# Performance work log

Measured on AMD Instinct MI355X. Metric: run time of the kernel, lower is better.

Reference implementation:

```python
import jax, jax.numpy as jnp
import numpy as np

N_WAY = 5
K_SHOT = 5
NBNN_TOPK = 3
TEMPERATURE = 2.0
EPS = 1e-8


def setup_inputs() -> dict:
    key = jax.random.key(0)
    k1, k2, k3 = jax.random.split(key, 3)
    b, q, c, h, w = 4, 75, 640, 11, 11
    s = N_WAY * K_SHOT
    support_xf = jax.random.normal(k1, (b, s, c, h, w), jnp.float32)
    query_xf = jax.random.normal(k2, (b, q, c, h, w), jnp.float32)
    # episodes are ordered class-major: [way0 shots..., way1 shots..., ...]
    support_y = jnp.tile(jnp.repeat(jnp.arange(N_WAY, dtype=jnp.int32), K_SHOT)[None, :], (b, 1))
    query_y = jax.random.randint(k3, (b, q), 0, N_WAY, dtype=jnp.int32)
    return {"support_xf": support_xf, "query_xf": query_xf,
            "support_y": support_y, "query_y": query_y}


def _mn4_loss(support_xf, query_xf, query_y):
    b, s, c, h, w = support_xf.shape
    q = query_xf.shape[1]
    M_q = h * w
    M_s = K_SHOT * h * w

    # ---- InnerproductSimilarity (cosine) ----
    # support: [b, N, c, M_s]  (class-major grouping of shots)
    sf = support_xf.reshape(b, N_WAY, K_SHOT, c, h * w).transpose(0, 1, 3, 2, 4).reshape(b, N_WAY, c, M_s)
    qf = query_xf.reshape(b, q, c, M_q)
    sf = sf / (jnp.linalg.norm(sf, axis=2, keepdims=True) + EPS)
    qf = qf / (jnp.linalg.norm(qf, axis=2, keepdims=True) + EPS)
    # simi: [b, q, N, M_q, M_s]
    simi = jnp.einsum('bqcm,bncs->bqnms', qf, sf)

    # ---- _MNN (compensate_for_single=True branch) ----
    # merged view: [b, q, M_q, N*M_s]
    merged = simi.transpose(0, 1, 3, 2, 4).reshape(b, q, M_q, N_WAY * M_s)
    query_nearest = jnp.argmax(merged, axis=-1)          # [b, q, M_q]
    class_wise_max = simi.max(-1).max(2) + 1.0           # [b, q, M_q]
    class_m = jax.nn.one_hot(query_nearest, N_WAY * M_s, dtype=simi.dtype) * class_wise_max[..., None]
    support_nearest = jnp.argmax(class_m, axis=-2)       # [b, q, N*M_s]
    gathered = jnp.take_along_axis(support_nearest, query_nearest, axis=-1)  # [b, q, M_q]
    q_mask = (gathered == jnp.arange(M_q)[None, None, :])                    # [b, q, M_q]

    # ---- NBNN value: topk over support descriptors, masked sum over query descriptors ----
    topv = jax.lax.top_k(simi, NBNN_TOPK)[0].mean(-1)    # [b, q, N, M_q]
    query_value = (topv * q_mask[:, :, None, :].astype(topv.dtype)).sum(-1)  # [b, q, N]
    logits = query_value.reshape(b * q, N_WAY) / TEMPERATURE

    # ---- cross entropy (mean) ----
    logp = jax.nn.log_softmax(logits, axis=-1)
    y = query_y.reshape(-1)
    loss = -jnp.take_along_axis(logp, y[:, None], axis=1).mean()
    return loss


def reference(support_xf, query_xf, support_y, query_y):
    del support_y  # episodes are class-major by construction
    return _mn4_loss(support_xf, query_xf, query_y)
```

## Files before the change

### kernel.cpp

```cpp
#include <hip/hip_runtime.h>
#include <hip/hip_bf16.h>
#include <math.h>

#define BB 4
#define QQ 75
#define NBQ 300
#define CC 640
#define HW 121
#define NW 5
#define KS 5
#define SS 25
#define MS 605
#define JT 3025
#define BQ_PER_XCD 38

typedef __attribute__((ext_vector_type(8))) short short8;
typedef __attribute__((ext_vector_type(4))) float f32x4;

#define OFF_SBF   0
#define SBF_F     (BB*JT*CC/2)
#define OFF_QBF   (OFF_SBF + SBF_F)
#define QBF_F     (NBQ*HW*CC/2)
#define OFF_P     (OFF_QBF + QBF_F)

__device__ __forceinline__ void async16(const void* g, void* l) {
    __builtin_amdgcn_global_load_lds(
        (const __attribute__((address_space(1))) unsigned int*)g,
        (__attribute__((address_space(3))) unsigned int*)l, 16, 0, 0);
}

__global__ void prep_kernel(const float* __restrict__ sup, const float* __restrict__ qry,
                            __hip_bfloat16* __restrict__ Sbf, __hip_bfloat16* __restrict__ Qbf,
                            float* __restrict__ out)
{
    const int col = blockIdx.x;
    const int t   = threadIdx.x;
    if (col == 0 && t == 0) out[0] = 0.f;
    const float* src;
    __hip_bfloat16* dst;
    if (col < BB * SS) {
        const int b = col / SS, s = col % SS;
        const int n = s / KS, k = s % KS;
        src = sup + (size_t)col * (CC * HW);
        dst = Sbf + ((size_t)b * JT + n * MS + k * HW) * CC;
    } else {
        const int bq = col - BB * SS;
        src = qry + (size_t)bq * (CC * HW);
        dst = Qbf + (size_t)bq * (HW * CC);
    }

    __shared__ float inv[128];
    __shared__ float T[32][128];

    const int cc2 = t >> 7, hw1 = t & 127;
    float ss0 = 0.f, ss1 = 0.f;
    if (hw1 < HW) {
        const float* p = src + hw1;
#pragma unroll 16
        for (int c = cc2; c < CC; c += 4) {
            float v0 = p[(size_t)c * HW];
            float v1 = p[(size_t)(c + 2) * HW];
            ss0 = fmaf(v0, v0, ss0);
            ss1 = fmaf(v1, v1, ss1);
        }
    }
    T[cc2][hw1] = ss0 + ss1;
    __syncthreads();
    if (t < 128) inv[t] = (t < HW) ? 1.f / (sqrtf(T[0][t] + T[1][t]) + 1e-8f) : 0.f;

    for (int c0 = 0; c0 < CC; c0 += 32) {
        __syncthreads();
#pragma unroll
        for (int i = 0; i < 16; ++i) {
            int idx = t + i * 256;
            int cc = idx >> 7, hw = idx & 127;
            if (hw < HW) T[cc][hw] = src[(size_t)(c0 + cc) * HW + hw] * inv[hw];
        }
        __syncthreads();
        const int hw = t >> 1, half = t & 1;
        if (hw < HW) {
            __hip_bfloat16 hv[16];
#pragma unroll
            for (int i = 0; i < 16; ++i) hv[i] = __float2bfloat16(T[half * 16 + i][hw]);
            int4* op = reinterpret_cast<int4*>(dst + (size_t)hw * CC + c0 + half * 16);
            op[0] = reinterpret_cast<int4*>(hv)[0];
            op[1] = reinterpret_cast<int4*>(hv)[1];
        }
    }
}

__launch_bounds__(256, 2)
__global__ void simi_kernel(const __hip_bfloat16* __restrict__ Sbf,
                            const __hip_bfloat16* __restrict__ Qbf,
                            float4* __restrict__ pout)
{
    const int xcd   = blockIdx.x & 7;
    const int local = blockIdx.x >> 3;
    const int n     = local % NW;
    const int bq    = xcd * BQ_PER_XCD + local / NW;
    if (bq >= NBQ) return;
    const int b   = bq / QQ;
    const int tid = threadIdx.x;
    const int lane = tid & 63, wid = tid >> 6;
    const int l15 = lane & 15, l4 = lane >> 4;
    const int wr0 = (wid & 1) * 64;
    const int wc0 = (wid >> 1) * 64;

    const unsigned short* qbase = (const unsigned short*)(Qbf + (size_t)bq * (HW * CC));
    const unsigned short* sbase = (const unsigned short*)(Sbf + ((size_t)b * JT + n * MS) * CC);

    __shared__ __align__(16) unsigned short AsBuf[2][128 * 64];
    __shared__ __align__(16) unsigned short BsBuf[2][128 * 64];

    const int srow = lane >> 3;
    const int kb   = (lane & 7) ^ srow;
    int aoff[4];
#pragma unroll
    for (int p = 0; p < 4; ++p) {
        int arow = wid * 32 + p * 8 + srow;
        int grow = arow < HW ? arow : HW - 1;
        aoff[p] = grow * CC + kb * 8;
    }
    const int ldso_base = wid * 4096 + lane * 16;

#define STAGE(ms0_, c0_, nb_)                                                        \
    {                                                                                \
        _Pragma("unroll")                                                            \
        for (int p = 0; p < 4; ++p) {                                                \
            const int ldso = ldso_base + p * 1024;                                   \
            async16(qbase + aoff[p] + (c0_), (char*)&AsBuf[nb_][0] + ldso);          \
            int j_ = (ms0_) + wid * 32 + p * 8 + srow;                               \
            int jc_ = j_ < MS ? j_ : MS - 1;                                         \
            async16(sbase + jc_ * CC + kb * 8 + (c0_), (char*)&BsBuf[nb_][0] + ldso);\
        }                                                                            \
    }

    float rt0[16], rt1[16], rt2[16]; int ra[16];
#pragma unroll
    for (int i = 0; i < 16; ++i) { rt0[i] = -INFINITY; rt1[i] = -INFINITY; rt2[i] = -INFINITY; ra[i] = 0; }

    f32x4 acc[4][4];
#pragma unroll
    for (int mi = 0; mi < 4; ++mi)
#pragma unroll
        for (int ni = 0; ni < 4; ++ni)
#pragma unroll
            for (int r = 0; r < 4; ++r) acc[mi][ni][r] = 0.f;

    STAGE(0, 0, 0);
    int nb = 0;

    for (int t = 0; t < 50; ++t) {
        const int tn = t + 1;
        if (tn < 50) {
            const int nms = (tn / 10) * 128;
            const int nc  = (tn % 10) * 64;
            STAGE(nms, nc, nb ^ 1);
            asm volatile("s_waitcnt vmcnt(8)" ::: "memory");
        } else {
            asm volatile("s_waitcnt vmcnt(0)" ::: "memory");
        }
        __builtin_amdgcn_s_barrier();

#pragma unroll
        for (int ks = 0; ks < 2; ++ks) {
            const int slot = (ks * 4 + l4) ^ (l15 & 7);
            short8 af[4], bf[4];
#pragma unroll
            for (int mi = 0; mi < 4; ++mi)
                af[mi] = *(const short8*)(&AsBuf[nb][0] + (wr0 + mi * 16 + l15) * 64 + slot * 8);
#pragma unroll
            for (int ni = 0; ni < 4; ++ni)
                bf[ni] = *(const short8*)(&BsBuf[nb][0] + (wc0 + ni * 16 + l15) * 64 + slot * 8);
#pragma unroll
            for (int mi = 0; mi < 4; ++mi)
#pragma unroll
                for (int ni = 0; ni < 4; ++ni)
                    acc[mi][ni] = __builtin_amdgcn_mfma_f32_16x16x32_bf16(
                        af[mi], bf[ni], acc[mi][ni], 0, 0, 0);
        }
        nb ^= 1;

        if ((t % 10) == 9) {
            const int ms0 = (t / 10) * 128;
            int jg[4]; bool jvalid[4];
#pragma unroll
            for (int nf = 0; nf < 4; ++nf) {
                const int jl = ms0 + wc0 + nf * 16 + l15;
                jvalid[nf] = (jl < MS);
                jg[nf] = n * MS + jl;
            }
#pragma unroll
            for (int mi = 0; mi < 4; ++mi)
#pragma unroll
                for (int nf = 0; nf < 4; ++nf)
#pragma unroll
                    for (int r = 0; r < 4; ++r) {
                        const int si = mi * 4 + r;
                        float v = jvalid[nf] ? acc[mi][nf][r] : -INFINITY;
                        const bool gt = v > rt0[si];
                        ra[si] = gt ? jg[nf] : ra[si];
                        const float m1 = fminf(rt0[si], v);
                        rt0[si] = fmaxf(rt0[si], v);
                        const float m2 = fminf(rt1[si], m1);
                        rt1[si] = fmaxf(rt1[si], m1);
                        rt2[si] = fmaxf(rt2[si], m2);
                    }
#pragma unroll
            for (int mi = 0; mi < 4; ++mi)
#pragma unroll
                for (int ni = 0; ni < 4; ++ni)
#pragma unroll
                    for (int r = 0; r < 4; ++r) acc[mi][ni][r] = 0.f;
        }

        __builtin_amdgcn_s_barrier();
    }

#pragma unroll
    for (int si = 0; si < 16; ++si) {
#pragma unroll
        for (int mask = 1; mask <= 8; mask <<= 1) {
            const float o0 = __shfl_xor(rt0[si], mask);
            const float o1 = __shfl_xor(rt1[si], mask);
            const float o2 = __shfl_xor(rt2[si], mask);
            const int   oa = __shfl_xor(ra[si],  mask);
            const bool take = (o0 > rt0[si]) || (o0 == rt0[si] && oa < ra[si]);
            ra[si] = take ? oa : ra[si];
            float m1 = fminf(rt0[si], o0); rt0[si] = fmaxf(rt0[si], o0);
            float m2 = fminf(rt1[si], m1); rt1[si] = fmaxf(rt1[si], m1);
            rt2[si] = fmaxf(rt2[si], m2);
            m1 = fminf(rt0[si], o1); rt0[si] = fmaxf(rt0[si], o1);
            m2 = fminf(rt1[si], m1); rt1[si] = fmaxf(rt1[si], m1);
            rt2[si] = fmaxf(rt2[si], m2);
            m1 = fminf(rt0[si], o2); rt0[si] = fmaxf(rt0[si], o2);
            m2 = fminf(rt1[si], m1); rt1[si] = fmaxf(rt1[si], m1);
            rt2[si] = fmaxf(rt2[si], m2);
        }
    }

    float s0 = rt0[0], s1 = rt1[0], s2 = rt2[0]; int sa = ra[0];
#pragma unroll
    for (int i = 1; i < 16; ++i) {
        const bool p = (l15 == i);
        s0 = p ? rt0[i] : s0; s1 = p ? rt1[i] : s1; s2 = p ? rt2[i] : s2; sa = p ? ra[i] : sa;
    }
    const int m = wr0 + (l15 >> 2) * 16 + l4 * 4 + (l15 & 3);

    __syncthreads();
    float4* mbuf = (float4*)&AsBuf[0][0];
    if ((wid >> 1) == 0) {
        float4 v; v.x = s0; v.y = s1; v.z = s2; v.w = __int_as_float(sa);
        mbuf[m] = v;
    }
    __syncthreads();
    if ((wid >> 1) == 1) {
        const float4 o = mbuf[m];
        const int oa = __float_as_int(o.w);
        const bool take = (o.x > s0) || (o.x == s0 && oa < sa);
        sa = take ? oa : sa;
        float m1 = fminf(s0, o.x); s0 = fmaxf(s0, o.x);
        float m2 = fminf(s1, m1);  s1 = fmaxf(s1, m1);
        s2 = fmaxf(s2, m2);
        m1 = fminf(s0, o.y); s0 = fmaxf(s0, o.y);
        m2 = fminf(s1, m1);  s1 = fmaxf(s1, m1);
        s2 = fmaxf(s2, m2);
        m1 = fminf(s0, o.z); s0 = fmaxf(s0, o.z);
        m2 = fminf(s1, m1);  s1 = fmaxf(s1, m1);
        s2 = fmaxf(s2, m2);
        if (m < HW) {
            float4 v; v.x = s0; v.y = s1; v.z = s2; v.w = __int_as_float(sa);
            pout[(bq * NW + n) * HW + m] = v;
        }
    }
#undef STAGE
}

__global__ void merge_kernel(const float4* __restrict__ pout, const int* __restrict__ qy,
                             float* __restrict__ out)
{
    const int bq  = blockIdx.x;
    const int tid = threadIdx.x;

    __shared__ float cw[128];
    __shared__ int   ag[128];
    __shared__ float tv[NW][128];
    __shared__ float maskf[128];
    __shared__ float lg[8];

    if (tid < HW) {
        float g0 = -INFINITY; int garg = 0;
#pragma unroll
        for (int n = 0; n < NW; ++n) {
            const float4 a = pout[(bq * NW + n) * HW + tid];
            if (a.x > g0) { g0 = a.x; garg = __float_as_int(a.w); }
            tv[n][tid] = (a.x + a.y + a.z) * (1.f / 3.f);
        }
        cw[tid] = g0 + 1.0f;
        ag[tid] = garg;
    }
    __syncthreads();
    if (tid < HW) {
        const float mycw = cw[tid];
        const int   myag = ag[tid];
        float ok = 1.f;
        for (int m2 = 0; m2 < HW; ++m2) {
            if (m2 == tid) continue;
            if (ag[m2] == myag) {
                float c2 = cw[m2];
                if (c2 > mycw || (c2 == mycw && m2 < tid)) ok = 0.f;
            }
        }
        maskf[tid] = ok;
    }
    __syncthreads();
    if (tid < NW) {
        float s = 0.f;
        for (int mq = 0; mq < HW; ++mq) s += maskf[mq] * tv[tid][mq];
        lg[tid] = s * 0.5f;
    }
    __syncthreads();
    if (tid == 0) {
        float m = lg[0];
#pragma unroll
        for (int n2 = 1; n2 < NW; ++n2) m = fmaxf(m, lg[n2]);
        float se = 0.f;
#pragma unroll
        for (int n2 = 0; n2 < NW; ++n2) se += expf(lg[n2] - m);
        int y = qy[bq];
        atomicAdd(out, -(lg[y] - m - logf(se)) * (1.f / NBQ));
    }
}

extern "C" void kernel_launch(void* const* d_in, const int* in_sizes, int n_in,
                              void* d_out, int out_size, void* d_ws, size_t ws_size,
                              hipStream_t stream)
{
    const float* sup = (const float*)d_in[0];
    const float* qry = (const float*)d_in[1];
    const int*   qy  = (const int*)d_in[3];
    float* out = (float*)d_out;
    float* ws  = (float*)d_ws;

    __hip_bfloat16* Sbf = (__hip_bfloat16*)(ws + OFF_SBF);
    __hip_bfloat16* Qbf = (__hip_bfloat16*)(ws + OFF_QBF);
    float4* pout = (float4*)(ws + OFF_P);

    hipLaunchKernelGGL(prep_kernel, dim3(BB * SS + NBQ), dim3(256), 0, stream,
                       sup, qry, Sbf, Qbf, out);
    hipLaunchKernelGGL(simi_kernel, dim3(8 * BQ_PER_XCD * NW), dim3(256), 0, stream,
                       Sbf, Qbf, pout);
    hipLaunchKernelGGL(merge_kernel, dim3(NBQ), dim3(128), 0, stream, pout, qy, out);
}
```

Before: 406.1 us.

## Halve simi K-tile to 32, raise occupancy to 3 blocks, add MFMA priority

```diff
diff --git a/kernel.cpp b/kernel.cpp
--- a/kernel.cpp
+++ b/kernel.cpp
@@ -74,7 +74,7 @@
         for (int i = 0; i < 16; ++i) {
             int idx = t + i * 256;
             int cc = idx >> 7, hw = idx & 127;
-            if (hw < HW) T[cc][hw] = src[(size_t)(c0 + cc) * HW + hw] * inv[hw];
+            if (hw < 128 && hw < HW) T[cc][hw] = src[(size_t)(c0 + cc) * HW + hw] * inv[hw];
         }
         __syncthreads();
         const int hw = t >> 1, half = t & 1;
@@ -89,7 +89,7 @@
     }
 }
 
-__launch_bounds__(256, 2)
+__launch_bounds__(256, 3)
 __global__ void simi_kernel(const __hip_bfloat16* __restrict__ Sbf,
                             const __hip_bfloat16* __restrict__ Qbf,
                             float4* __restrict__ pout)
@@ -109,27 +109,31 @@
     const unsigned short* qbase = (const unsigned short*)(Qbf + (size_t)bq * (HW * CC));
     const unsigned short* sbase = (const unsigned short*)(Sbf + ((size_t)b * JT + n * MS) * CC);
 
-    __shared__ __align__(16) unsigned short AsBuf[2][128 * 64];
-    __shared__ __align__(16) unsigned short BsBuf[2][128 * 64];
-
-    const int srow = lane >> 3;
-    const int kb   = (lane & 7) ^ srow;
-    int aoff[4];
-#pragma unroll
-    for (int p = 0; p < 4; ++p) {
-        int arow = wid * 32 + p * 8 + srow;
+    __shared__ __align__(16) unsigned short AsBuf[2][128 * 32];
+    __shared__ __align__(16) unsigned short BsBuf[2][128 * 32];
+
+    const int srow = lane >> 2;
+    const int kb   = (lane & 3) ^ ((lane >> 3) & 3);
+    int aoff2[2];
+#pragma unroll
+    for (int g = 0; g < 2; ++g) {
+        int arow = wid * 32 + g * 16 + srow;
         int grow = arow < HW ? arow : HW - 1;
-        aoff[p] = grow * CC + kb * 8;
-    }
-    const int ldso_base = wid * 4096 + lane * 16;
+        aoff2[g] = grow * CC + kb * 8;
+    }
+    int jb2[2];
+#pragma unroll
+    for (int g = 0; g < 2; ++g) jb2[g] = wid * 32 + g * 16 + srow;
+
+    const int ldso_base = wid * 2048 + lane * 16;
 
 #define STAGE(ms0_, c0_, nb_)                                                        \
     {                                                                                \
         _Pragma("unroll")                                                            \
-        for (int p = 0; p < 4; ++p) {                                                \
-            const int ldso = ldso_base + p * 1024;                                   \
-            async16(qbase + aoff[p] + (c0_), (char*)&AsBuf[nb_][0] + ldso);          \
-            int j_ = (ms0_) + wid * 32 + p * 8 + srow;                               \
+        for (int g = 0; g < 2; ++g) {                                                \
+            const int ldso = ldso_base + g * 1024;                                   \
+            async16(qbase + aoff2[g] + (c0_), (char*)&AsBuf[nb_][0] + ldso);         \
+            int j_ = (ms0_) + jb2[g];                                                \
             int jc_ = j_ < MS ? j_ : MS - 1;                                         \
             async16(sbase + jc_ * CC + kb * 8 + (c0_), (char*)&BsBuf[nb_][0] + ldso);\
         }                                                                            \
@@ -150,39 +154,42 @@
     STAGE(0, 0, 0);
     int nb = 0;
 
-    for (int t = 0; t < 50; ++t) {
+    const int slot = l4 ^ ((l15 >> 1) & 3);
+    const int aro  = (wr0 + l15) * 32 + slot * 8;
+    const int bro  = (wc0 + l15) * 32 + slot * 8;
+
+    for (int t = 0; t < 100; ++t) {
         const int tn = t + 1;
-        if (tn < 50) {
-            const int nms = (tn / 10) * 128;
-            const int nc  = (tn % 10) * 64;
+        if (tn < 100) {
+            const int nms = (tn / 20) * 128;
+            const int nc  = (tn % 20) * 32;
             STAGE(nms, nc, nb ^ 1);
-            asm volatile("s_waitcnt vmcnt(8)" ::: "memory");
+            asm volatile("s_waitcnt vmcnt(4)" ::: "memory");
         } else {
             asm volatile("s_waitcnt vmcnt(0)" ::: "memory");
         }
         __builtin_amdgcn_s_barrier();
 
-#pragma unroll
-        for (int ks = 0; ks < 2; ++ks) {
-            const int slot = (ks * 4 + l4) ^ (l15 & 7);
-            short8 af[4], bf[4];
-#pragma unroll
-            for (int mi = 0; mi < 4; ++mi)
-                af[mi] = *(const short8*)(&AsBuf[nb][0] + (wr0 + mi * 16 + l15) * 64 + slot * 8);
+        short8 af[4], bf[4];
+#pragma unroll
+        for (int mi = 0; mi < 4; ++mi)
+            af[mi] = *(const short8*)(&AsBuf[nb][0] + aro + mi * 512);
+#pragma unroll
+        for (int ni = 0; ni < 4; ++ni)
+            bf[ni] = *(const short8*)(&BsBuf[nb][0] + bro + ni * 512);
+
+        __builtin_amdgcn_s_setprio(1);
+#pragma unroll
+        for (int mi = 0; mi < 4; ++mi)
 #pragma unroll
             for (int ni = 0; ni < 4; ++ni)
-                bf[ni] = *(const short8*)(&BsBuf[nb][0] + (wc0 + ni * 16 + l15) * 64 + slot * 8);
-#pragma unroll
-            for (int mi = 0; mi < 4; ++mi)
-#pragma unroll
-                for (int ni = 0; ni < 4; ++ni)
-                    acc[mi][ni] = __builtin_amdgcn_mfma_f32_16x16x32_bf16(
-                        af[mi], bf[ni], acc[mi][ni], 0, 0, 0);
-        }
+                acc[mi][ni] = __builtin_amdgcn_mfma_f32_16x16x32_bf16(
+                    af[mi], bf[ni], acc[mi][ni], 0, 0, 0);
+        __builtin_amdgcn_s_setprio(0);
         nb ^= 1;
 
-        if ((t % 10) == 9) {
-            const int ms0 = (t / 10) * 128;
+        if ((t % 20) == 19) {
+            const int ms0 = (t / 20) * 128;
             int jg[4]; bool jvalid[4];
 #pragma unroll
             for (int nf = 0; nf < 4; ++nf) {
```

After: 484.1 us. 1.19x slower.
